# Performance work log

Hardware: AMD Instinct MI355X
Metric: run time of the kernel (lower is better)

Reference implementation:

```python
import jax, jax.numpy as jnp
import numpy as np

N = 100000
E = 1600000


def gcn_conv(x, W, b, src, dst, n):
    # PyG GCNConv: h = x @ W, symmetric normalization with self-loops, then + b
    h = x @ W  # [N, out]
    ones = jnp.ones(src.shape, dtype=h.dtype)
    deg = jax.ops.segment_sum(ones, dst, num_segments=n)  # in-degree incl self-loops
    dinv = jnp.where(deg > 0, jax.lax.rsqrt(deg), 0.0)
    norm = dinv[src] * dinv[dst]  # [E]
    msg = h[src] * norm[:, None]  # gather + scale
    out = jax.ops.segment_sum(msg, dst, num_segments=n)  # scatter-add
    return out + b


def setup_inputs() -> dict:
    key = jax.random.key(0)
    k1, k2, k3, k4 = jax.random.split(key, 4)
    x = jax.random.normal(k1, (N, 128), dtype=jnp.float32)
    edge_index = jax.random.randint(k2, (2, E), 0, N, dtype=jnp.int64)
    # Glorot-ish init for weights
    W1 = jax.random.normal(k3, (128, 64), dtype=jnp.float32) / np.sqrt(128.0)
    b1 = jnp.zeros((64,), dtype=jnp.float32)
    W2 = jax.random.normal(k4, (64, 64), dtype=jnp.float32) / np.sqrt(64.0)
    b2 = jnp.zeros((64,), dtype=jnp.float32)
    return {"x": x, "edge_index": edge_index, "W1": W1, "b1": b1, "W2": W2, "b2": b2}


def reference(x, edge_index, W1, b1, W2, b2):
    n = x.shape[0]
    loops = jnp.arange(n, dtype=edge_index.dtype)
    src = jnp.concatenate([edge_index[0], loops])  # add self-loops (GCNConv default)
    dst = jnp.concatenate([edge_index[1], loops])
    h = jax.nn.relu(gcn_conv(x, W1, b1, src, dst, n))
    out = gcn_conv(h, W2, b2, src, dst, n)
    return out
```

## Files before the change

kernel.cpp:

```cpp
#include <hip/hip_runtime.h>


#define GSB 2048

__global__ __launch_bounds__(256) void detect_dtype_kernel(const unsigned* __restrict__ w,
                                                           int E, unsigned* __restrict__ flag) {
  __shared__ unsigned sacc;
  if (threadIdx.x == 0) sacc = 0u;
  __syncthreads();
  int ns = min(16384, E);
  unsigned acc = 0;
  for (int i = threadIdx.x; i < ns; i += 256) acc |= w[2 * i + 1];
  if (__any(acc != 0) && (threadIdx.x & 63) == 0) sacc = 1u;
  __syncthreads();
  if (threadIdx.x == 0) *flag = sacc;
}

__device__ __forceinline__ int edge_src(const int* w, long e, long E, bool is64) {
  return is64 ? w[2 * e] : w[e];
}
__device__ __forceinline__ int edge_dst(const int* w, long e, long E, bool is64) {
  return is64 ? w[2 * (E + e)] : w[E + e];
}

__global__ __launch_bounds__(256) void count_deg_kernel(const int* __restrict__ w, int E,
                                                        const unsigned* __restrict__ flag,
                                                        int* __restrict__ cnt) {
  bool is64 = (*flag == 0u);
  int stride = gridDim.x * blockDim.x;
  for (int e = blockIdx.x * blockDim.x + threadIdx.x; e < E; e += stride)
    atomicAdd(&cnt[edge_dst(w, e, E, is64)], 1);
}

#define SCAN_BS 256
__global__ void scan_block_kernel(const int* __restrict__ cnt, int n, int* __restrict__ bsums) {
  __shared__ int s[SCAN_BS];
  int gid = blockIdx.x * SCAN_BS + threadIdx.x;
  s[threadIdx.x] = (gid < n) ? cnt[gid] : 0;
  __syncthreads();
  for (int st = SCAN_BS / 2; st > 0; st >>= 1) {
    if (threadIdx.x < st) s[threadIdx.x] += s[threadIdx.x + st];
    __syncthreads();
  }
  if (threadIdx.x == 0) bsums[blockIdx.x] = s[0];
}

__global__ __launch_bounds__(512) void scan_bsums_kernel(int* __restrict__ bsums, int nb) {
  __shared__ int s[512];
  int carry = 0;
  for (int base = 0; base < nb; base += 512) {
    int g = base + threadIdx.x;
    int v = (g < nb) ? bsums[g] : 0;
    s[threadIdx.x] = v;
    __syncthreads();
    for (int st = 1; st < 512; st <<= 1) {
      int t = (threadIdx.x >= st) ? s[threadIdx.x - st] : 0;
      __syncthreads();
      s[threadIdx.x] += t;
      __syncthreads();
    }
    if (g < nb) bsums[g] = carry + s[threadIdx.x] - v;
    carry += s[511];
    __syncthreads();
  }
}

__global__ void scan_apply_kernel(const int* __restrict__ cnt, int n,
                                  const int* __restrict__ bsums, int* __restrict__ offs,
                                  float* __restrict__ dinv, int E) {
  __shared__ int s[SCAN_BS];
  int gid = blockIdx.x * SCAN_BS + threadIdx.x;
  int v = (gid < n) ? cnt[gid] : 0;
  s[threadIdx.x] = v;
  __syncthreads();
  for (int st = 1; st < SCAN_BS; st <<= 1) {
    int t = (threadIdx.x >= st) ? s[threadIdx.x - st] : 0;
    __syncthreads();
    s[threadIdx.x] += t;
    __syncthreads();
  }
  if (gid < n) {
    offs[gid] = bsums[blockIdx.x] + s[threadIdx.x] - v;
    dinv[gid] = rsqrtf((float)v + 1.0f);
    if (gid == n - 1) offs[n] = E;
  }
}

__global__ void build_csr_kernel(const int* __restrict__ w, int E,
                                 const unsigned* __restrict__ flag,
                                 const int* __restrict__ offs, int* __restrict__ fill,
                                 const float* __restrict__ dinv,
                                 int2* __restrict__ csr) {
  bool is64 = (*flag == 0u);
  int stride = gridDim.x * blockDim.x;
  for (int e = blockIdx.x * blockDim.x + threadIdx.x; e < E; e += stride) {
    int s = edge_src(w, e, E, is64);
    int d = edge_dst(w, e, E, is64);
    int pos = offs[d] + atomicAdd(&fill[d], 1);
    int2 rec;
    rec.x = s;
    rec.y = __float_as_int(dinv[s] * dinv[d]);
    csr[pos] = rec;
  }
}

template <int K>
__global__ __launch_bounds__(256) void gemm_kernel(const float* __restrict__ X,
                                                   const float* __restrict__ W,
                                                   float* __restrict__ H, int n) {
  __shared__ float Ws[K * 64];
  for (int i = threadIdx.x; i < K * 64; i += 256) Ws[i] = W[i];
  __syncthreads();
  int row = blockIdx.x * 256 + threadIdx.x;
  if (row >= n) return;
  const float4* xr = (const float4*)(X + (size_t)row * K);
  float acc[64];
#pragma unroll
  for (int c = 0; c < 64; c++) acc[c] = 0.f;
#pragma unroll 4
  for (int k4 = 0; k4 < K / 4; k4++) {
    float4 xv = xr[k4];
#pragma unroll
    for (int kk = 0; kk < 4; kk++) {
      float xs = (kk == 0) ? xv.x : (kk == 1) ? xv.y : (kk == 2) ? xv.z : xv.w;
      const float4* wr = (const float4*)&Ws[(k4 * 4 + kk) * 64];
#pragma unroll
      for (int c4 = 0; c4 < 16; c4++) {
        float4 wv = wr[c4];
        acc[c4 * 4 + 0] += xs * wv.x;
        acc[c4 * 4 + 1] += xs * wv.y;
        acc[c4 * 4 + 2] += xs * wv.z;
        acc[c4 * 4 + 3] += xs * wv.w;
      }
    }
  }
  float4* ho = (float4*)(H + (size_t)row * 64);
#pragma unroll
  for (int c4 = 0; c4 < 16; c4++) {
    float4 v;
    v.x = acc[c4 * 4 + 0]; v.y = acc[c4 * 4 + 1];
    v.z = acc[c4 * 4 + 2]; v.w = acc[c4 * 4 + 3];
    ho[c4] = v;
  }
}

__global__ __launch_bounds__(256) void aggregate_kernel(
    const float4* __restrict__ H4, const int* __restrict__ offs,
    const int2* __restrict__ csr,
    const float* __restrict__ dinv, const float4* __restrict__ bias4,
    float4* __restrict__ OUT4, int n, int relu) {
  int wid = (blockIdx.x * 256 + threadIdx.x) >> 6;
  int lane = threadIdx.x & 63;
  if (wid >= n) return;
  int grp = lane >> 4;
  int fl = lane & 15;
  int beg = offs[wid];
  int end = offs[wid + 1];
  float4 acc = {0.f, 0.f, 0.f, 0.f};
  for (int base = beg; base < end; base += 64) {
    int m = min(64, end - base);
    int sl = 0; float nl = 0.f;
    if (lane < m) {
      int2 rec = csr[base + lane];
      sl = rec.x;
      nl = __int_as_float(rec.y);
    }
    int iters = ((m + 31) >> 5) << 3;
    for (int j0 = 0; j0 < iters; j0 += 8) {
      int s[8]; float w[8]; float4 h[8];
#pragma unroll
      for (int t = 0; t < 8; t++) {
        int idx = (j0 + t) * 4 + grp;
        s[t] = __shfl(sl, idx);
        w[t] = __shfl(nl, idx);
      }
#pragma unroll
      for (int t = 0; t < 8; t++) h[t] = H4[(size_t)s[t] * 16 + fl];
#pragma unroll
      for (int t = 0; t < 8; t++) {
        acc.x += h[t].x * w[t];
        acc.y += h[t].y * w[t];
        acc.z += h[t].z * w[t];
        acc.w += h[t].w * w[t];
      }
    }
  }
#pragma unroll
  for (int off2 = 32; off2 >= 16; off2 >>= 1) {
    acc.x += __shfl_xor(acc.x, off2);
    acc.y += __shfl_xor(acc.y, off2);
    acc.z += __shfl_xor(acc.z, off2);
    acc.w += __shfl_xor(acc.w, off2);
  }
  if (lane < 16) {
    float di = dinv[wid];
    float d2 = di * di;
    float4 hv = H4[(size_t)wid * 16 + fl];
    float4 bv = bias4[fl];
    acc.x += hv.x * d2 + bv.x;
    acc.y += hv.y * d2 + bv.y;
    acc.z += hv.z * d2 + bv.z;
    acc.w += hv.w * d2 + bv.w;
    if (relu) {
      acc.x = fmaxf(acc.x, 0.f);
      acc.y = fmaxf(acc.y, 0.f);
      acc.z = fmaxf(acc.z, 0.f);
      acc.w = fmaxf(acc.w, 0.f);
    }
    OUT4[(size_t)wid * 16 + fl] = acc;
  }
}

extern "C" void kernel_launch(void* const* d_in, const int* in_sizes, int n_in,
                              void* d_out, int out_size, void* d_ws, size_t ws_size,
                              hipStream_t stream) {
  const float* x  = (const float*)d_in[0];
  const int*   ei = (const int*)d_in[1];
  const float* W1 = (const float*)d_in[2];
  const float* b1 = (const float*)d_in[3];
  const float* W2 = (const float*)d_in[4];
  const float* b2 = (const float*)d_in[5];
  float* out = (float*)d_out;

  const int N = in_sizes[0] / 128;
  const int E = in_sizes[1] / 2;

  size_t off = 0;
  char* base = (char*)d_ws;
  auto alloc = [&](size_t bytes) -> void* {
    void* p = base + off;
    off += (bytes + 255) & ~(size_t)255;
    return p;
  };
  int*      cnt  = (int*)alloc((size_t)N * 4);
  int*      fill = (int*)alloc((size_t)N * 4);
  unsigned* flag = (unsigned*)alloc(256);
  size_t zero_bytes = off;
  int*   offs  = (int*)alloc((size_t)(N + 1) * 4);
  float* dinv  = (float*)alloc((size_t)N * 4);
  int nb = (N + SCAN_BS - 1) / SCAN_BS;
  int*   bsums = (int*)alloc((size_t)nb * 4);
  int2*  csr   = (int2*)alloc((size_t)E * 8);
  float* h1    = (float*)alloc((size_t)N * 64 * 4);
  float* a1    = (float*)alloc((size_t)N * 64 * 4);
  float* h2    = h1;

  hipMemsetAsync(d_ws, 0, zero_bytes, stream);

  int gemm_blocks = (N + 255) / 256;
  int agg_blocks = (N + 3) / 4;

  detect_dtype_kernel<<<1, 256, 0, stream>>>((const unsigned*)ei, E, flag);
  count_deg_kernel<<<GSB, 256, 0, stream>>>(ei, E, flag, cnt);
  scan_block_kernel<<<nb, SCAN_BS, 0, stream>>>(cnt, N, bsums);
  scan_bsums_kernel<<<1, 512, 0, stream>>>(bsums, nb);
  scan_apply_kernel<<<nb, SCAN_BS, 0, stream>>>(cnt, N, bsums, offs, dinv, E);
  build_csr_kernel<<<GSB, 256, 0, stream>>>(ei, E, flag, offs, fill, dinv, csr);

  gemm_kernel<128><<<gemm_blocks, 256, 0, stream>>>(x, W1, h1, N);
  aggregate_kernel<<<agg_blocks, 256, 0, stream>>>(
      (const float4*)h1, offs, csr, dinv, (const float4*)b1, (float4*)a1, N, 1);

  gemm_kernel<64><<<gemm_blocks, 256, 0, stream>>>(a1, W2, h2, N);
  aggregate_kernel<<<agg_blocks, 256, 0, stream>>>(
      (const float4*)h2, offs, csr, dinv, (const float4*)b2, (float4*)out, N, 0);
}
```

Baseline: 434.7 us.

## Store hidden features in fp16 and fuse layer-1 aggregation with second GEMM

The intermediate feature matrices h1 and h2 are now stored as fp16. This halves the bytes moved by the random-gather aggregation. The first aggregation kernel also applies bias and ReLU and then multiplies by W2 inside the wave via shuffles, which removes the a1 round trip and one GEMM launch. The trade-off is reduced precision in the gathered features and extra shuffle/LDS work per node in the fused kernel.

```diff
diff --git a/kernel.cpp b/kernel.cpp
--- a/kernel.cpp
+++ b/kernel.cpp
@@ -1,7 +1,14 @@
 #include <hip/hip_runtime.h>
+#include <hip/hip_fp16.h>
 
 
 #define GSB 2048
+#define SCAN_BS 256
+
+__device__ __forceinline__ float h2f(unsigned short u) {
+  __half_raw r; r.x = u;
+  return __half2float((__half)r);
+}
 
 __global__ __launch_bounds__(256) void detect_dtype_kernel(const unsigned* __restrict__ w,
                                                            int E, unsigned* __restrict__ flag) {
@@ -32,7 +39,6 @@
     atomicAdd(&cnt[edge_dst(w, e, E, is64)], 1);
 }
 
-#define SCAN_BS 256
 __global__ void scan_block_kernel(const int* __restrict__ cnt, int n, int* __restrict__ bsums) {
   __shared__ int s[SCAN_BS];
   int gid = blockIdx.x * SCAN_BS + threadIdx.x;
@@ -104,21 +110,20 @@
   }
 }
 
-template <int K>
-__global__ __launch_bounds__(256) void gemm_kernel(const float* __restrict__ X,
-                                                   const float* __restrict__ W,
-                                                   float* __restrict__ H, int n) {
-  __shared__ float Ws[K * 64];
-  for (int i = threadIdx.x; i < K * 64; i += 256) Ws[i] = W[i];
+__global__ __launch_bounds__(256) void gemm1_kernel(const float* __restrict__ X,
+                                                    const float* __restrict__ W,
+                                                    __half* __restrict__ H, int n) {
+  __shared__ float Ws[128 * 64];
+  for (int i = threadIdx.x; i < 128 * 64; i += 256) Ws[i] = W[i];
   __syncthreads();
   int row = blockIdx.x * 256 + threadIdx.x;
   if (row >= n) return;
-  const float4* xr = (const float4*)(X + (size_t)row * K);
+  const float4* xr = (const float4*)(X + (size_t)row * 128);
   float acc[64];
 #pragma unroll
   for (int c = 0; c < 64; c++) acc[c] = 0.f;
 #pragma unroll 4
-  for (int k4 = 0; k4 < K / 4; k4++) {
+  for (int k4 = 0; k4 < 32; k4++) {
     float4 xv = xr[k4];
 #pragma unroll
     for (int kk = 0; kk < 4; kk++) {
@@ -136,26 +141,19 @@
   }
   float4* ho = (float4*)(H + (size_t)row * 64);
 #pragma unroll
-  for (int c4 = 0; c4 < 16; c4++) {
-    float4 v;
-    v.x = acc[c4 * 4 + 0]; v.y = acc[c4 * 4 + 1];
-    v.z = acc[c4 * 4 + 2]; v.w = acc[c4 * 4 + 3];
-    ho[c4] = v;
-  }
-}
-
-__global__ __launch_bounds__(256) void aggregate_kernel(
-    const float4* __restrict__ H4, const int* __restrict__ offs,
-    const int2* __restrict__ csr,
-    const float* __restrict__ dinv, const float4* __restrict__ bias4,
-    float4* __restrict__ OUT4, int n, int relu) {
-  int wid = (blockIdx.x * 256 + threadIdx.x) >> 6;
-  int lane = threadIdx.x & 63;
-  if (wid >= n) return;
-  int grp = lane >> 4;
-  int fl = lane & 15;
-  int beg = offs[wid];
-  int end = offs[wid + 1];
+  for (int g = 0; g < 8; g++) {
+    union { __half2 h[4]; float4 f; } u;
+    u.h[0] = __floats2half2_rn(acc[8 * g + 0], acc[8 * g + 1]);
+    u.h[1] = __floats2half2_rn(acc[8 * g + 2], acc[8 * g + 3]);
+    u.h[2] = __floats2half2_rn(acc[8 * g + 4], acc[8 * g + 5]);
+    u.h[3] = __floats2half2_rn(acc[8 * g + 6], acc[8 * g + 7]);
+    ho[g] = u.f;
+  }
+}
+
+__device__ __forceinline__ float4 gather_row(
+    const ushort4* __restrict__ H16, const int2* __restrict__ csr,
+    int beg, int end, int lane, int grp, int fl) {
   float4 acc = {0.f, 0.f, 0.f, 0.f};
   for (int base = beg; base < end; base += 64) {
     int m = min(64, end - base);
@@ -167,7 +165,7 @@
     }
     int iters = ((m + 31) >> 5) << 3;
     for (int j0 = 0; j0 < iters; j0 += 8) {
-      int s[8]; float w[8]; float4 h[8];
+      int s[8]; float w[8]; ushort4 h[8];
 #pragma unroll
       for (int t = 0; t < 8; t++) {
         int idx = (j0 + t) * 4 + grp;
@@ -175,13 +173,13 @@
         w[t] = __shfl(nl, idx);
       }
 #pragma unroll
-      for (int t = 0; t < 8; t++) h[t] = H4[(size_t)s[t] * 16 + fl];
+      for (int t = 0; t < 8; t++) h[t] = H16[(size_t)s[t] * 16 + fl];
 #pragma unroll
       for (int t = 0; t < 8; t++) {
-        acc.x += h[t].x * w[t];
-        acc.y += h[t].y * w[t];
-        acc.z += h[t].z * w[t];
-        acc.w += h[t].w * w[t];
+        acc.x += h2f(h[t].x) * w[t];
+        acc.y += h2f(h[t].y) * w[t];
+        acc.z += h2f(h[t].z) * w[t];
+        acc.w += h2f(h[t].w) * w[t];
       }
     }
   }
@@ -192,21 +190,64 @@
     acc.z += __shfl_xor(acc.z, off2);
     acc.w += __shfl_xor(acc.w, off2);
   }
+  return acc;
+}
+
+__global__ __launch_bounds__(256) void agg1_gemm2_kernel(
+    const ushort4* __restrict__ H16, const int* __restrict__ offs,
+    const int2* __restrict__ csr, const float* __restrict__ dinv,
+    const float4* __restrict__ b1_4, const float* __restrict__ W2,
+    __half* __restrict__ H2, int n) {
+  __shared__ float W2s[64 * 64];
+  for (int i = threadIdx.x; i < 64 * 64; i += 256) W2s[i] = W2[i];
+  __syncthreads();
+  int wid = (blockIdx.x * 256 + threadIdx.x) >> 6;
+  int lane = threadIdx.x & 63;
+  if (wid >= n) return;
+  int grp = lane >> 4, fl = lane & 15;
+  float4 acc = gather_row(H16, csr, offs[wid], offs[wid + 1], lane, grp, fl);
+  float di = dinv[wid];
+  float d2 = di * di;
+  ushort4 hv = H16[(size_t)wid * 16 + fl];
+  float4 bv = b1_4[fl];
+  float4 av;
+  av.x = fmaxf(acc.x + h2f(hv.x) * d2 + bv.x, 0.f);
+  av.y = fmaxf(acc.y + h2f(hv.y) * d2 + bv.y, 0.f);
+  av.z = fmaxf(acc.z + h2f(hv.z) * d2 + bv.z, 0.f);
+  av.w = fmaxf(acc.w + h2f(hv.w) * d2 + bv.w, 0.f);
+  float o = 0.f;
+#pragma unroll
+  for (int k16 = 0; k16 < 16; k16++) {
+    float a0 = __shfl(av.x, k16);
+    float a1 = __shfl(av.y, k16);
+    float a2 = __shfl(av.z, k16);
+    float a3 = __shfl(av.w, k16);
+    o += a0 * W2s[(k16 * 4 + 0) * 64 + lane];
+    o += a1 * W2s[(k16 * 4 + 1) * 64 + lane];
+    o += a2 * W2s[(k16 * 4 + 2) * 64 + lane];
+    o += a3 * W2s[(k16 * 4 + 3) * 64 + lane];
+  }
+  H2[(size_t)wid * 64 + lane] = __float2half(o);
+}
+
+__global__ __launch_bounds__(256) void agg2_kernel(
+    const ushort4* __restrict__ H16, const int* __restrict__ offs,
+    const int2* __restrict__ csr, const float* __restrict__ dinv,
+    const float4* __restrict__ b2_4, float4* __restrict__ OUT4, int n) {
+  int wid = (blockIdx.x * 256 + threadIdx.x) >> 6;
+  int lane = threadIdx.x & 63;
+  if (wid >= n) return;
+  int grp = lane >> 4, fl = lane & 15;
+  float4 acc = gather_row(H16, csr, offs[wid], offs[wid + 1], lane, grp, fl);
   if (lane < 16) {
     float di = dinv[wid];
     float d2 = di * di;
-    float4 hv = H4[(size_t)wid * 16 + fl];
-    float4 bv = bias4[fl];
-    acc.x += hv.x * d2 + bv.x;
-    acc.y += hv.y * d2 + bv.y;
-    acc.z += hv.z * d2 + bv.z;
-    acc.w += hv.w * d2 + bv.w;
-    if (relu) {
-      acc.x = fmaxf(acc.x, 0.f);
-      acc.y = fmaxf(acc.y, 0.f);
-      acc.z = fmaxf(acc.z, 0.f);
-      acc.w = fmaxf(acc.w, 0.f);
-    }
+    ushort4 hv = H16[(size_t)wid * 16 + fl];
+    float4 bv = b2_4[fl];
+    acc.x += h2f(hv.x) * d2 + bv.x;
+    acc.y += h2f(hv.y) * d2 + bv.y;
+    acc.z += h2f(hv.z) * d2 + bv.z;
+    acc.w += h2f(hv.w) * d2 + bv.w;
     OUT4[(size_t)wid * 16 + fl] = acc;
   }
 }
@@ -241,9 +282,8 @@
   int nb = (N + SCAN_BS - 1) / SCAN_BS;
   int*   bsums = (int*)alloc((size_t)nb * 4);
   int2*  csr   = (int2*)alloc((size_t)E * 8);
-  float* h1    = (float*)alloc((size_t)N * 64 * 4);
-  float* a1    = (float*)alloc((size_t)N * 64 * 4);
-  float* h2    = h1;
+  __half* h1   = (__half*)alloc((size_t)N * 64 * 2);
+  __half* h2   = (__half*)alloc((size_t)N * 64 * 2);
 
   hipMemsetAsync(d_ws, 0, zero_bytes, stream);
 
@@ -257,11 +297,10 @@
   scan_apply_kernel<<<nb, SCAN_BS, 0, stream>>>(cnt, N, bsums, offs, dinv, E);
   build_csr_kernel<<<GSB, 256, 0, stream>>>(ei, E, flag, offs, fill, dinv, csr);
 
-  gemm_kernel<128><<<gemm_blocks, 256, 0, stream>>>(x, W1, h1, N);
-  aggregate_kernel<<<agg_blocks, 256, 0, stream>>>(
-      (const float4*)h1, offs, csr, dinv, (const float4*)b1, (float4*)a1, N, 1);
-
-  gemm_kernel<64><<<gemm_blocks, 256, 0, stream>>>(a1, W2, h2, N);
-  aggregate_kernel<<<agg_blocks, 256, 0, stream>>>(
-      (const float4*)h2, offs, csr, dinv, (const float4*)b2, (float4*)out, N, 0);
-}
+  gemm1_kernel<<<gemm_blocks, 256, 0, stream>>>(x, W1, h1, N);
+  agg1_gemm2_kernel<<<agg_blocks, 256, 0, stream>>>(
+      (const ushort4*)h1, offs, csr, dinv, (const float4*)b1, W2, h2, N);
+
+  agg2_kernel<<<agg_blocks, 256, 0, stream>>>(
+      (const ushort4*)h2, offs, csr, dinv, (const float4*)b2, (float4*)out, N);
+}
```

After: 453.5 us. 1.04x slower.

## Build CSR via destination-bucket binning with LDS fill counters

Applied to the files above, without the earlier changes.

Replaces the degree-count and global-atomic CSR build with a two-pass binning scheme. The first pass counts degrees and also scatters (src,dst) pairs into per-bucket, per-color cells. A per-bucket place kernel then assigns CSR positions using shared-memory fill counters. The aim is to cut global atomic contention and the scattered CSR writes and second edge read of the old build. The cost is extra atomics on cell counters, a fixed-capacity bin buffer aliased with the feature buffers, and an overflow path capped at OVF_CAP that silently drops edges if exceeded.

```diff
diff --git a/kernel.cpp b/kernel.cpp
--- a/kernel.cpp
+++ b/kernel.cpp
@@ -2,6 +2,11 @@
 
 
 #define GSB 2048
+#define SCAN_BS 256
+#define COLORS 8
+#define BUCKET_NODES 256
+#define CELL_CAP 1024
+#define OVF_CAP 4096
 
 __global__ __launch_bounds__(256) void detect_dtype_kernel(const unsigned* __restrict__ w,
                                                            int E, unsigned* __restrict__ flag) {
@@ -23,16 +28,25 @@
   return is64 ? w[2 * (E + e)] : w[E + e];
 }
 
-__global__ __launch_bounds__(256) void count_deg_kernel(const int* __restrict__ w, int E,
-                                                        const unsigned* __restrict__ flag,
-                                                        int* __restrict__ cnt) {
+__global__ __launch_bounds__(256) void binpass_kernel(
+    const int* __restrict__ w, int E, const unsigned* __restrict__ flag,
+    int* __restrict__ cnt, int* __restrict__ cellCnt, int2* __restrict__ bins,
+    int2* __restrict__ ovf, int* __restrict__ ovfCnt) {
   bool is64 = (*flag == 0u);
+  int color = blockIdx.x & (COLORS - 1);
   int stride = gridDim.x * blockDim.x;
-  for (int e = blockIdx.x * blockDim.x + threadIdx.x; e < E; e += stride)
-    atomicAdd(&cnt[edge_dst(w, e, E, is64)], 1);
-}
-
-#define SCAN_BS 256
+  for (int e = blockIdx.x * blockDim.x + threadIdx.x; e < E; e += stride) {
+    int s = edge_src(w, e, E, is64);
+    int d = edge_dst(w, e, E, is64);
+    atomicAdd(&cnt[d], 1);
+    int cell = (d >> 8) * COLORS + color;
+    int p = atomicAdd(&cellCnt[cell], 1);
+    int2 rec; rec.x = s; rec.y = d;
+    if (p < CELL_CAP) bins[(size_t)cell * CELL_CAP + p] = rec;
+    else { int q = atomicAdd(ovfCnt, 1); if (q < OVF_CAP) ovf[q] = rec; }
+  }
+}
+
 __global__ void scan_block_kernel(const int* __restrict__ cnt, int n, int* __restrict__ bsums) {
   __shared__ int s[SCAN_BS];
   int gid = blockIdx.x * SCAN_BS + threadIdx.x;
@@ -86,21 +100,41 @@
   }
 }
 
-__global__ void build_csr_kernel(const int* __restrict__ w, int E,
-                                 const unsigned* __restrict__ flag,
-                                 const int* __restrict__ offs, int* __restrict__ fill,
-                                 const float* __restrict__ dinv,
-                                 int2* __restrict__ csr) {
-  bool is64 = (*flag == 0u);
-  int stride = gridDim.x * blockDim.x;
-  for (int e = blockIdx.x * blockDim.x + threadIdx.x; e < E; e += stride) {
-    int s = edge_src(w, e, E, is64);
-    int d = edge_dst(w, e, E, is64);
-    int pos = offs[d] + atomicAdd(&fill[d], 1);
-    int2 rec;
-    rec.x = s;
-    rec.y = __float_as_int(dinv[s] * dinv[d]);
-    csr[pos] = rec;
+__global__ __launch_bounds__(256) void place_kernel(
+    const int2* __restrict__ bins, const int* __restrict__ cellCnt,
+    const int2* __restrict__ ovf, const int* __restrict__ ovfCnt,
+    const int* __restrict__ offs, const float* __restrict__ dinv,
+    int2* __restrict__ csr) {
+  __shared__ int lfill[BUCKET_NODES];
+  int b = blockIdx.x;
+  int node0 = b * BUCKET_NODES;
+  for (int i = threadIdx.x; i < BUCKET_NODES; i += 256) lfill[i] = 0;
+  __syncthreads();
+  for (int c = 0; c < COLORS; c++) {
+    int cell = b * COLORS + c;
+    int m = min(cellCnt[cell], CELL_CAP);
+    const int2* seg = bins + (size_t)cell * CELL_CAP;
+    for (int i = threadIdx.x; i < m; i += 256) {
+      int2 rec = seg[i];
+      int d = rec.y;
+      int pos = offs[d] + atomicAdd(&lfill[d - node0], 1);
+      int2 out;
+      out.x = rec.x;
+      out.y = __float_as_int(dinv[rec.x] * dinv[d]);
+      csr[pos] = out;
+    }
+  }
+  int q = min(*ovfCnt, OVF_CAP);
+  for (int i = threadIdx.x; i < q; i += 256) {
+    int2 rec = ovf[i];
+    int d = rec.y;
+    if (d >= node0 && d < node0 + BUCKET_NODES) {
+      int pos = offs[d] + atomicAdd(&lfill[d - node0], 1);
+      int2 out;
+      out.x = rec.x;
+      out.y = __float_as_int(dinv[rec.x] * dinv[d]);
+      csr[pos] = out;
+    }
   }
 }
 
@@ -224,6 +258,8 @@
 
   const int N = in_sizes[0] / 128;
   const int E = in_sizes[1] / 2;
+  const int nbuck = (N + BUCKET_NODES - 1) / BUCKET_NODES;
+  const int ncells = nbuck * COLORS;
 
   size_t off = 0;
   char* base = (char*)d_ws;
@@ -232,18 +268,25 @@
     off += (bytes + 255) & ~(size_t)255;
     return p;
   };
-  int*      cnt  = (int*)alloc((size_t)N * 4);
-  int*      fill = (int*)alloc((size_t)N * 4);
-  unsigned* flag = (unsigned*)alloc(256);
+  int*      cnt     = (int*)alloc((size_t)N * 4);
+  unsigned* flag    = (unsigned*)alloc(256);
+  int*      cellCnt = (int*)alloc((size_t)ncells * 4);
+  int*      ovfCnt  = (int*)alloc(256);
   size_t zero_bytes = off;
   int*   offs  = (int*)alloc((size_t)(N + 1) * 4);
   float* dinv  = (float*)alloc((size_t)N * 4);
   int nb = (N + SCAN_BS - 1) / SCAN_BS;
   int*   bsums = (int*)alloc((size_t)nb * 4);
   int2*  csr   = (int2*)alloc((size_t)E * 8);
-  float* h1    = (float*)alloc((size_t)N * 64 * 4);
-  float* a1    = (float*)alloc((size_t)N * 64 * 4);
-  float* h2    = h1;
+  int2*  ovf   = (int2*)alloc((size_t)OVF_CAP * 8);
+  size_t feat_bytes = (size_t)N * 64 * 4;
+  size_t bins_bytes = (size_t)ncells * CELL_CAP * 8;
+  size_t region = bins_bytes > 2 * feat_bytes ? bins_bytes : 2 * feat_bytes;
+  char* R = (char*)alloc(region);
+  int2*  bins = (int2*)R;
+  float* h1   = (float*)R;
+  float* a1   = (float*)(R + feat_bytes);
+  float* h2   = h1;
 
   hipMemsetAsync(d_ws, 0, zero_bytes, stream);
 
@@ -251,11 +294,11 @@
   int agg_blocks = (N + 3) / 4;
 
   detect_dtype_kernel<<<1, 256, 0, stream>>>((const unsigned*)ei, E, flag);
-  count_deg_kernel<<<GSB, 256, 0, stream>>>(ei, E, flag, cnt);
+  binpass_kernel<<<GSB, 256, 0, stream>>>(ei, E, flag, cnt, cellCnt, bins, ovf, ovfCnt);
   scan_block_kernel<<<nb, SCAN_BS, 0, stream>>>(cnt, N, bsums);
   scan_bsums_kernel<<<1, 512, 0, stream>>>(bsums, nb);
   scan_apply_kernel<<<nb, SCAN_BS, 0, stream>>>(cnt, N, bsums, offs, dinv, E);
-  build_csr_kernel<<<GSB, 256, 0, stream>>>(ei, E, flag, offs, fill, dinv, csr);
+  place_kernel<<<nbuck, 256, 0, stream>>>(bins, cellCnt, ovf, ovfCnt, offs, dinv, csr);
 
   gemm_kernel<128><<<gemm_blocks, 256, 0, stream>>>(x, W1, h1, N);
   aggregate_kernel<<<agg_blocks, 256, 0, stream>>>(
```

Result: slower. 527.5 us (+21.3%).

## Build CSR via two-level bucketed counting sort with shared-memory atomics

Applied to the files above, without the earlier changes.

Replaces the global-atomic degree count and CSR fill with a bucket sort. Edges are first scattered into 128-destination buckets by 64 chunk blocks using shared-memory histograms, then per-bucket kernels count degrees and place records using local atomics. The aim is to remove random global atomics and scattered writes, at the cost of more kernel launches, a padded intermediate array, and only 64 blocks in the scatter phases, which limits parallelism.

```diff
diff --git a/kernel.cpp b/kernel.cpp
--- a/kernel.cpp
+++ b/kernel.cpp
@@ -1,7 +1,12 @@
 #include <hip/hip_runtime.h>
 
 
-#define GSB 2048
+#define NB_SCAT 64
+#define BUCKET 128
+#define PADREC 16
+#define SCAN_BS 256
+#define INVALID_BIT (1u << 27)
+#define SRC_MASK 0xFFFFFu
 
 __global__ __launch_bounds__(256) void detect_dtype_kernel(const unsigned* __restrict__ w,
                                                            int E, unsigned* __restrict__ flag) {
@@ -16,23 +21,30 @@
   if (threadIdx.x == 0) *flag = sacc;
 }
 
-__device__ __forceinline__ int edge_src(const int* w, long e, long E, bool is64) {
-  return is64 ? w[2 * e] : w[e];
-}
-__device__ __forceinline__ int edge_dst(const int* w, long e, long E, bool is64) {
-  return is64 ? w[2 * (E + e)] : w[E + e];
-}
-
-__global__ __launch_bounds__(256) void count_deg_kernel(const int* __restrict__ w, int E,
-                                                        const unsigned* __restrict__ flag,
-                                                        int* __restrict__ cnt) {
+__device__ __forceinline__ int edge_src(const int* w, int e, int E, bool is64) {
+  return is64 ? w[2 * (long)e] : w[e];
+}
+__device__ __forceinline__ int edge_dst(const int* w, int e, int E, bool is64) {
+  return is64 ? w[2 * ((long)E + e)] : w[(long)E + e];
+}
+
+__global__ __launch_bounds__(256) void histA_kernel(const int* __restrict__ w, int E,
+                                                    const unsigned* __restrict__ flag,
+                                                    int nbuck, int* __restrict__ hist) {
+  __shared__ int h[1024];
   bool is64 = (*flag == 0u);
-  int stride = gridDim.x * blockDim.x;
-  for (int e = blockIdx.x * blockDim.x + threadIdx.x; e < E; e += stride)
-    atomicAdd(&cnt[edge_dst(w, e, E, is64)], 1);
-}
-
-#define SCAN_BS 256
+  int i = blockIdx.x;
+  int CH = (E + NB_SCAT - 1) / NB_SCAT;
+  int e0 = i * CH, e1 = min(E, e0 + CH);
+  for (int b = threadIdx.x; b < nbuck; b += 256) h[b] = 0;
+  __syncthreads();
+  for (int e = e0 + threadIdx.x; e < e1; e += 256)
+    atomicAdd(&h[edge_dst(w, e, E, is64) >> 7], 1);
+  __syncthreads();
+  for (int b = threadIdx.x; b < nbuck; b += 256)
+    hist[b * NB_SCAT + i] = (h[b] + PADREC - 1) & ~(PADREC - 1);
+}
+
 __global__ void scan_block_kernel(const int* __restrict__ cnt, int n, int* __restrict__ bsums) {
   __shared__ int s[SCAN_BS];
   int gid = blockIdx.x * SCAN_BS + threadIdx.x;
@@ -66,8 +78,8 @@
 }
 
 __global__ void scan_apply_kernel(const int* __restrict__ cnt, int n,
-                                  const int* __restrict__ bsums, int* __restrict__ offs,
-                                  float* __restrict__ dinv, int E) {
+                                  const int* __restrict__ bsums, int* __restrict__ out,
+                                  float* __restrict__ dinv) {
   __shared__ int s[SCAN_BS];
   int gid = blockIdx.x * SCAN_BS + threadIdx.x;
   int v = (gid < n) ? cnt[gid] : 0;
@@ -80,26 +92,79 @@
     __syncthreads();
   }
   if (gid < n) {
-    offs[gid] = bsums[blockIdx.x] + s[threadIdx.x] - v;
-    dinv[gid] = rsqrtf((float)v + 1.0f);
-    if (gid == n - 1) offs[n] = E;
-  }
-}
-
-__global__ void build_csr_kernel(const int* __restrict__ w, int E,
-                                 const unsigned* __restrict__ flag,
-                                 const int* __restrict__ offs, int* __restrict__ fill,
-                                 const float* __restrict__ dinv,
-                                 int2* __restrict__ csr) {
+    int ex = bsums[blockIdx.x] + s[threadIdx.x] - v;
+    out[gid] = ex;
+    if (dinv) dinv[gid] = rsqrtf((float)v + 1.0f);
+    if (gid == n - 1) out[n] = ex + v;
+  }
+}
+
+__global__ __launch_bounds__(256) void scatter_kernel(const int* __restrict__ w, int E,
+                                                      const unsigned* __restrict__ flag,
+                                                      int nbuck, const int* __restrict__ shist,
+                                                      unsigned* __restrict__ arr) {
+  __shared__ int cur[1024];
   bool is64 = (*flag == 0u);
-  int stride = gridDim.x * blockDim.x;
-  for (int e = blockIdx.x * blockDim.x + threadIdx.x; e < E; e += stride) {
+  int i = blockIdx.x;
+  for (int b = threadIdx.x; b < nbuck; b += 256) cur[b] = shist[b * NB_SCAT + i];
+  __syncthreads();
+  int CH = (E + NB_SCAT - 1) / NB_SCAT;
+  int e0 = i * CH, e1 = min(E, e0 + CH);
+  for (int e = e0 + threadIdx.x; e < e1; e += 256) {
     int s = edge_src(w, e, E, is64);
     int d = edge_dst(w, e, E, is64);
-    int pos = offs[d] + atomicAdd(&fill[d], 1);
+    int p = atomicAdd(&cur[d >> 7], 1);
+    arr[p] = (unsigned)s | ((unsigned)(d & 127) << 20);
+  }
+  __syncthreads();
+  for (int b = threadIdx.x; b < nbuck; b += 256) {
+    int endp = shist[b * NB_SCAT + i + 1];
+    for (int p = cur[b]; p < endp; p++) arr[p] = INVALID_BIT;
+  }
+}
+
+__global__ __launch_bounds__(256) void degcnt_kernel(const unsigned* __restrict__ arr,
+                                                     const int* __restrict__ shist,
+                                                     int N, int* __restrict__ cnt) {
+  __shared__ int c[BUCKET];
+  int b = blockIdx.x;
+  for (int t = threadIdx.x; t < BUCKET; t += 256) c[t] = 0;
+  __syncthreads();
+  int eb = shist[b * NB_SCAT], ee = shist[(b + 1) * NB_SCAT];
+  for (int p = eb + threadIdx.x; p < ee; p += 256) {
+    unsigned r = arr[p];
+    if (!(r & INVALID_BIT)) atomicAdd(&c[(r >> 20) & 127], 1);
+  }
+  __syncthreads();
+  int g = b * BUCKET + threadIdx.x;
+  if (threadIdx.x < BUCKET && g < N) cnt[g] = c[threadIdx.x];
+}
+
+__global__ __launch_bounds__(256) void place_kernel(
+    const unsigned* __restrict__ arr, const int* __restrict__ shist,
+    const int* __restrict__ offs, const float* __restrict__ dinv,
+    int N, int2* __restrict__ csr) {
+  __shared__ int lfill[BUCKET];
+  __shared__ int loffs[BUCKET];
+  __shared__ float dl[BUCKET];
+  int b = blockIdx.x, d0 = b * BUCKET;
+  for (int t = threadIdx.x; t < BUCKET; t += 256) {
+    lfill[t] = 0;
+    int g = d0 + t;
+    loffs[t] = (g < N) ? offs[g] : 0;
+    dl[t] = (g < N) ? dinv[g] : 0.f;
+  }
+  __syncthreads();
+  int eb = shist[b * NB_SCAT], ee = shist[(b + 1) * NB_SCAT];
+  for (int p = eb + threadIdx.x; p < ee; p += 256) {
+    unsigned r = arr[p];
+    if (r & INVALID_BIT) continue;
+    int s = r & SRC_MASK;
+    int dloc = (r >> 20) & 127;
+    int pos = loffs[dloc] + atomicAdd(&lfill[dloc], 1);
     int2 rec;
     rec.x = s;
-    rec.y = __float_as_int(dinv[s] * dinv[d]);
+    rec.y = __float_as_int(dinv[s] * dl[dloc]);
     csr[pos] = rec;
   }
 }
@@ -224,6 +289,8 @@
 
   const int N = in_sizes[0] / 128;
   const int E = in_sizes[1] / 2;
+  const int nbuck = (N + BUCKET - 1) / BUCKET;
+  const int L = nbuck * NB_SCAT;
 
   size_t off = 0;
   char* base = (char*)d_ws;
@@ -232,18 +299,21 @@
     off += (bytes + 255) & ~(size_t)255;
     return p;
   };
-  int*      cnt  = (int*)alloc((size_t)N * 4);
-  int*      fill = (int*)alloc((size_t)N * 4);
-  unsigned* flag = (unsigned*)alloc(256);
+  unsigned* flag  = (unsigned*)alloc(256);
   size_t zero_bytes = off;
-  int*   offs  = (int*)alloc((size_t)(N + 1) * 4);
-  float* dinv  = (float*)alloc((size_t)N * 4);
-  int nb = (N + SCAN_BS - 1) / SCAN_BS;
-  int*   bsums = (int*)alloc((size_t)nb * 4);
-  int2*  csr   = (int2*)alloc((size_t)E * 8);
-  float* h1    = (float*)alloc((size_t)N * 64 * 4);
-  float* a1    = (float*)alloc((size_t)N * 64 * 4);
-  float* h2    = h1;
+  int*      hist  = (int*)alloc((size_t)L * 4);
+  int*      shist = (int*)alloc((size_t)(L + 1) * 4);
+  int*      cnt   = (int*)alloc((size_t)N * 4);
+  int*      offs  = (int*)alloc((size_t)(N + 1) * 4);
+  float*    dinv  = (float*)alloc((size_t)N * 4);
+  int nb1 = (L + SCAN_BS - 1) / SCAN_BS;
+  int nb2 = (N + SCAN_BS - 1) / SCAN_BS;
+  int*      bsums = (int*)alloc((size_t)(nb1 > nb2 ? nb1 : nb2) * 4);
+  unsigned* arr   = (unsigned*)alloc(((size_t)E + (size_t)PADREC * L) * 4);
+  int2*     csr   = (int2*)alloc((size_t)E * 8);
+  float*    h1    = (float*)alloc((size_t)N * 64 * 4);
+  float*    a1    = (float*)alloc((size_t)N * 64 * 4);
+  float*    h2    = h1;
 
   hipMemsetAsync(d_ws, 0, zero_bytes, stream);
 
@@ -251,11 +321,16 @@
   int agg_blocks = (N + 3) / 4;
 
   detect_dtype_kernel<<<1, 256, 0, stream>>>((const unsigned*)ei, E, flag);
-  count_deg_kernel<<<GSB, 256, 0, stream>>>(ei, E, flag, cnt);
-  scan_block_kernel<<<nb, SCAN_BS, 0, stream>>>(cnt, N, bsums);
-  scan_bsums_kernel<<<1, 512, 0, stream>>>(bsums, nb);
-  scan_apply_kernel<<<nb, SCAN_BS, 0, stream>>>(cnt, N, bsums, offs, dinv, E);
-  build_csr_kernel<<<GSB, 256, 0, stream>>>(ei, E, flag, offs, fill, dinv, csr);
+  histA_kernel<<<NB_SCAT, 256, 0, stream>>>(ei, E, flag, nbuck, hist);
+  scan_block_kernel<<<nb1, SCAN_BS, 0, stream>>>(hist, L, bsums);
+  scan_bsums_kernel<<<1, 512, 0, stream>>>(bsums, nb1);
+  scan_apply_kernel<<<nb1, SCAN_BS, 0, stream>>>(hist, L, bsums, shist, nullptr);
+  scatter_kernel<<<NB_SCAT, 256, 0, stream>>>(ei, E, flag, nbuck, shist, arr);
+  degcnt_kernel<<<nbuck, 256, 0, stream>>>(arr, shist, N, cnt);
+  scan_block_kernel<<<nb2, SCAN_BS, 0, stream>>>(cnt, N, bsums);
+  scan_bsums_kernel<<<1, 512, 0, stream>>>(bsums, nb2);
+  scan_apply_kernel<<<nb2, SCAN_BS, 0, stream>>>(cnt, N, bsums, offs, dinv);
+  place_kernel<<<nbuck, 256, 0, stream>>>(arr, shist, offs, dinv, N, csr);
 
   gemm_kernel<128><<<gemm_blocks, 256, 0, stream>>>(x, W1, h1, N);
   aggregate_kernel<<<agg_blocks, 256, 0, stream>>>(
```

Result: faster. 405.0 us (-6.8%).
